# Optimization experiments

Measured on AMD Instinct MI355X. Metric: run time of the kernel, lower is better.

The kernel has to match this reference:

```python
import jax, jax.numpy as jnp
from jax import lax
import numpy as np

CH = 16
STAGES = 6
DN = ('NDHWC', 'DHWIO', 'NDHWC')


def setup_inputs() -> dict:
    key = jax.random.key(0)
    ks = jax.random.split(key, 16)
    B, G = 8, 64
    x = jax.random.normal(ks[0], (B, G, G, G, 1), dtype=jnp.float32)
    mask = jax.random.randint(ks[1], (B, G, G, G), 0, 2, dtype=jnp.int32)
    meta = jax.random.normal(ks[2], (B, 3), dtype=jnp.float32)
    sched = jax.random.normal(ks[3], (B, 128), dtype=jnp.float32)
    s = 0.05
    w_stem = jax.random.normal(ks[4], (5, 5, 5, 1, CH), dtype=jnp.float32) * s
    w_stages = jax.random.normal(ks[5], (STAGES, 3, 3, 3, CH, CH), dtype=jnp.float32) * s
    meta_w1 = jax.random.normal(ks[6], (3, 32), dtype=jnp.float32) * s
    meta_b1 = jnp.zeros((32,), jnp.float32)
    meta_w2 = jax.random.normal(ks[7], (32, 16), dtype=jnp.float32) * s
    meta_b2 = jnp.zeros((16,), jnp.float32)
    mat_w = jax.random.normal(ks[8], (CH * STAGES + 16, 128), dtype=jnp.float32) * s
    mat_b = jnp.zeros((128,), jnp.float32)
    sch_w = jax.random.normal(ks[9], (128, 128), dtype=jnp.float32) * s
    sch_b = jnp.zeros((128,), jnp.float32)
    f1_w = jax.random.normal(ks[10], (256, 128), dtype=jnp.float32) * s
    f1_b = jnp.zeros((128,), jnp.float32)
    f2_w = jax.random.normal(ks[11], (128, 1), dtype=jnp.float32) * s
    f2_b = jnp.zeros((1,), jnp.float32)
    return dict(x=x, mask=mask, meta=meta, sched=sched, w_stem=w_stem,
                w_stages=w_stages, meta_w1=meta_w1, meta_b1=meta_b1,
                meta_w2=meta_w2, meta_b2=meta_b2, mat_w=mat_w, mat_b=mat_b,
                sch_w=sch_w, sch_b=sch_b, f1_w=f1_w, f1_b=f1_b,
                f2_w=f2_w, f2_b=f2_b)


def _pool_mask(m):
    # ME stride-2 output coords = unique(coords // 2): 2x2x2 max-pool, ceil sizes
    return lax.reduce_window(m, jnp.float32(0), lax.max,
                             (1, 2, 2, 2), (1, 2, 2, 2), 'SAME')


def reference(x, mask, meta, sched, w_stem, w_stages, meta_w1, meta_b1,
              meta_w2, meta_b2, mat_w, mat_b, sch_w, sch_b,
              f1_w, f1_b, f2_w, f2_b):
    m = mask.astype(x.dtype)
    feats = x * m[..., None]                       # zero features off-mask
    y = lax.conv_general_dilated(feats, w_stem, (1, 1, 1), 'SAME',
                                 dimension_numbers=DN)
    y = jnp.maximum(y * m[..., None], 0.0)         # stem: conv + mask + ReLU
    pools = []
    for i in range(STAGES):
        y = lax.conv_general_dilated(y, w_stages[i], (2, 2, 2),
                                     [(1, 1), (1, 1), (1, 1)],
                                     dimension_numbers=DN)
        m = _pool_mask(m)
        y = jnp.maximum(y * m[..., None], 0.0)
        denom = jnp.maximum(m.sum(axis=(1, 2, 3)), 1.0)   # occupied voxels
        pools.append(y.sum(axis=(1, 2, 3)) / denom[:, None])
    pools = jnp.concatenate(pools, axis=1)                 # [B, CH*STAGES]
    h = jax.nn.relu(meta[:, :3] @ meta_w1 + meta_b1)
    meta_emb = h @ meta_w2 + meta_b2                        # [B,16]
    m_emb = jax.nn.relu(jnp.concatenate([pools, meta_emb], 1) @ mat_w + mat_b)
    s_emb = jax.nn.relu(sched @ sch_w + sch_b)
    z = jnp.concatenate([m_emb, s_emb], axis=1)             # [B,256]
    z = jax.nn.relu(z @ f1_w + f1_b)
    return z @ f2_w + f2_b                                  # [B,1]
```

## Files before the change

### kernel.cpp

```cpp
#include <hip/hip_runtime.h>

#define CH 16
#define NB 8

typedef unsigned short u16;
typedef unsigned char u8;
typedef unsigned int u32;
typedef __attribute__((ext_vector_type(8))) short s16x8;
typedef __attribute__((ext_vector_type(4))) float f32x4;

__device__ __forceinline__ float bflo(u32 u) { return __uint_as_float(u << 16); }
__device__ __forceinline__ float bfhi(u32 u) { return __uint_as_float(u & 0xffff0000u); }
__device__ __forceinline__ u32 bfrnd(float f) {
  u32 u = __float_as_uint(f);
  return (u + 0x7fffu + ((u >> 16) & 1u)) >> 16;
}
__device__ __forceinline__ u32 packbf_hw(float lo, float hi) {
  u32 r;
  asm("v_cvt_pk_bf16_f32 %0, %1, %2" : "=v"(r) : "v"(lo), "v"(hi));
  return r;
}

__global__ __launch_bounds__(256) void bprep_kernel(
    const float* __restrict__ w_stg, const float* __restrict__ w_stem,
    u16* __restrict__ bpre)
{
  const int e = blockIdx.x * 256 + (int)threadIdx.x;
  if (e >= 4 * 7168 + 3584) return;
  if (e < 4 * 7168) {
    const int s = e / 7168, r0 = e % 7168;
    const int i = r0 >> 9;
    const int r = r0 & 511;
    const int l = r >> 3, j = r & 7;
    const int tap = 2 * i + (l >> 5);
    const int cin = ((l >> 4) & 1) * 8 + j;
    const int n = l & 15;
    const float* w = w_stg + s * 27 * 256;
    const float val = (tap < 27) ? w[(tap * 16 + cin) * 16 + n] : 0.f;
    bpre[s * 7168 + i * 512 + l * 8 + j] = (u16)bfrnd(val);
  } else {
    const int e2 = e - 4 * 7168;
    const int i = e2 >> 9;
    const int r0 = e2 & 511;
    const int lane = r0 >> 3, j = r0 & 7;
    const int quad = lane >> 4, n = lane & 15;
    const int r = i * 4 + quad;
    const float val = (r < 25 && j < 5) ? w_stem[(r * 5 + j) * 16 + n] : 0.f;
    bpre[4 * 7168 + e2] = (u16)bfrnd(val);
  }
}

__global__ __launch_bounds__(256, 6) void stem_mfma(
    const float* __restrict__ x, const int* __restrict__ mask,
    const u16* __restrict__ bpre, u16* __restrict__ yout,
    float* __restrict__ pool_sum, float* __restrict__ cnt)
{
  __shared__ u16 cp[8 * 1168];

  const int b = blockIdx.y;
  const int u = blockIdx.x;
  const int tb = ((u & 7) << 6) | (u >> 3);
  const int z0 = (tb >> 6) * 8;
  const int y0 = ((tb >> 3) & 7) * 8;
  const int x0 = (tb & 7) * 8;
  const int tid = threadIdx.x;

  if (tb == 0) {
    if (tid < 96) pool_sum[b * 96 + tid] = 0.f;
    else if (tid < 102) cnt[b * 6 + (tid - 96)] = 0.f;
  }

  const int lane = tid & 63;
  const int wv = tid >> 6;
  const int n = lane & 15;
  const int quad = lane >> 4;
  const int vy = n >> 2, vx = n & 3;

  s16x8 wf[7];
  {
    const s16x8* wfp = (const s16x8*)(bpre + 4 * 7168);
#pragma unroll
    for (int i = 0; i < 7; ++i) wf[i] = wfp[i * 64 + lane];
  }

  if (tid < 144) {
    const int lz = tid / 12, ly = tid - lz * 12;
    const int gz = z0 + lz - 2, gy = y0 + ly - 2;
    uint4* dst = (uint4*)&cp[tid * 8];
    if ((unsigned)gz < 64u && (unsigned)gy < 64u) {
      const long long rowg =
          ((long long)((b * 64 + gz) * 64 + gy)) * 64 + (x0 - 2);
      float v[12];
      if (rowg >= 0 && rowg + 12 <= (long long)NB * 64 * 64 * 64) {
        const float2* xp = (const float2*)(x + rowg);
        const int2* mp2 = (const int2*)(mask + rowg);
        float2 xv[6]; int2 mv2[6];
#pragma unroll
        for (int j = 0; j < 6; ++j) { xv[j] = xp[j]; mv2[j] = mp2[j]; }
#pragma unroll
        for (int j = 0; j < 6; ++j) {
          v[2 * j]     = xv[j].x * (float)mv2[j].x;
          v[2 * j + 1] = xv[j].y * (float)mv2[j].y;
        }
        if (x0 == 0)  { v[0] = 0.f;  v[1] = 0.f;  }
        if (x0 == 56) { v[10] = 0.f; v[11] = 0.f; }
      } else {
#pragma unroll
        for (int j = 0; j < 12; ++j) {
          const int gx = x0 - 2 + j;
          float vv = 0.f;
          if ((unsigned)gx < 64u) {
            const long long gi = rowg + j;
            vv = x[gi] * (float)mask[gi];
          }
          v[j] = vv;
        }
      }
      const u32 c0 = packbf_hw(v[0], v[1]);
      const u32 c1 = packbf_hw(v[2], v[3]);
      const u32 c2 = packbf_hw(v[4], v[5]);
      const u32 c3 = packbf_hw(v[6], v[7]);
      const u32 c4 = packbf_hw(v[8], v[9]);
      const u32 c5 = packbf_hw(v[10], v[11]);
      const u32 d0 = packbf_hw(v[1], v[2]);
      const u32 d1 = packbf_hw(v[3], v[4]);
      const u32 d2 = packbf_hw(v[5], v[6]);
      const u32 d3 = packbf_hw(v[7], v[8]);
      const u32 d4 = packbf_hw(v[9], v[10]);
      const u32 d5 = packbf_hw(v[11], 0.f);
      dst[0 * 146] = make_uint4(c0, c1, c2, c3);
      dst[1 * 146] = make_uint4(d0, d1, d2, d3);
      dst[2 * 146] = make_uint4(c1, c2, c3, c4);
      dst[3 * 146] = make_uint4(d1, d2, d3, d4);
      dst[4 * 146] = make_uint4(c2, c3, c4, c5);
      dst[5 * 146] = make_uint4(d2, d3, d4, d5);
      dst[6 * 146] = make_uint4(c3, c4, c5, 0u);
      dst[7 * 146] = make_uint4(d3, d4, d5, 0u);
    } else {
#pragma unroll
      for (int p = 0; p < 8; ++p) dst[p * 146] = make_uint4(0u, 0u, 0u, 0u);
    }
  }
  __syncthreads();

  int doff[7];
#pragma unroll
  for (int i = 0; i < 7; ++i) {
    const int r = i * 4 + quad;
    doff[i] = (r < 25) ? ((r / 5) * 12 + (r % 5)) * 8 : 0;
  }
  const int base0 = vx * 1168 + (wv * 12 + vy) * 8;
  const int gi0 = ((b * 64 + z0 + wv) * 64 + y0 + vy) * 64 + x0 + vx;
  u16* outp = yout + (size_t)gi0 * 16 + quad * 4;

  float mvc = (float)mask[gi0];
  for (int s = 0; s < 8; ++s) {
    const int sz = (s >> 2) * 4, sy2 = ((s >> 1) & 1) * 4, sx = (s & 1) * 4;
    const int off = sz * 4096 + sy2 * 64 + sx;
    float mvn = 0.f;
    if (s < 7) {
      const int s1 = s + 1;
      const int offn = ((s1 >> 2) * 4) * 4096 + (((s1 >> 1) & 1) * 4) * 64 +
                       (s1 & 1) * 4;
      mvn = (float)mask[gi0 + offn];
    }
    const int base = base0 + sx * 1168 + (sz * 12 + sy2) * 8;
    f32x4 accA = {0.f, 0.f, 0.f, 0.f};
    f32x4 accB = {0.f, 0.f, 0.f, 0.f};
#pragma unroll
    for (int i = 0; i < 7; ++i) {
      const s16x8 bf = *(const s16x8*)&cp[base + doff[i]];
      if (i & 1)
        accB = __builtin_amdgcn_mfma_f32_16x16x32_bf16(wf[i], bf, accB, 0, 0, 0);
      else
        accA = __builtin_amdgcn_mfma_f32_16x16x32_bf16(wf[i], bf, accA, 0, 0, 0);
    }
    const float f0 = fmaxf(accA[0] + accB[0], 0.f) * mvc;
    const float f1 = fmaxf(accA[1] + accB[1], 0.f) * mvc;
    const float f2 = fmaxf(accA[2] + accB[2], 0.f) * mvc;
    const float f3 = fmaxf(accA[3] + accB[3], 0.f) * mvc;
    *(uint2*)(outp + (size_t)off * 16) =
        make_uint2(packbf_hw(f0, f1), packbf_hw(f2, f3));
    mvc = mvn;
  }
}

template <int S>
__global__ __launch_bounds__(256) void stage_mfma4(
    const u16* __restrict__ yin, const u16* __restrict__ bpre,
    const int* __restrict__ m_in_i, const u8* __restrict__ m_in_u8,
    u16* __restrict__ yout, u8* __restrict__ m_out,
    float* __restrict__ pool_sum, float* __restrict__ cnt,
    const int stage)
{
  __shared__ u16 lb[14 * 512];
  __shared__ float lmp[256];
  __shared__ float lps[4][16];

  constexpr int So = S >> 1;
  constexpr int nvox = So * So * So;
  constexpr int NBX = nvox / 256;
  const int b = blockIdx.y;
  const int tid = threadIdx.x;
  const int u = blockIdx.x;
  int bxi;
  if constexpr (NBX >= 8) bxi = (u & 7) * (NBX / 8) + (u >> 3);
  else bxi = u;
  const int vg0 = bxi * 256;

  {
    const uint4* src = (const uint4*)bpre;
    uint4* dst = (uint4*)lb;
    for (int e = tid; e < 896; e += 256) dst[e] = src[e];
  }

  {
    const int vox = vg0 + tid;
    const int oz = vox / (So * So);
    const int oy = (vox / So) % So;
    const int ox = vox % So;
    float mp = 0.f;
#pragma unroll
    for (int dz = 0; dz < 2; ++dz)
#pragma unroll
      for (int dy = 0; dy < 2; ++dy)
#pragma unroll
        for (int dx = 0; dx < 2; ++dx) {
          const int mi =
              ((b * S + 2 * oz + dz) * S + 2 * oy + dy) * S + 2 * ox + dx;
          const float mv = m_in_i ? (float)m_in_i[mi] : (float)m_in_u8[mi];
          mp = fmaxf(mp, mv);
        }
    lmp[tid] = mp;
  }
  __syncthreads();

  const int wv = tid >> 6;
  const int lane = tid & 63;
  const int m = lane & 15;
  const int quad = lane >> 4;
  const int qh = quad >> 1;
  const int qlo = quad & 1;

  int izb[4], iyb[4], ixb[4];
#pragma unroll
  for (int g = 0; g < 4; ++g) {
    const int vox = vg0 + wv * 64 + g * 16 + m;
    const int oz = vox / (So * So);
    const int oy = (vox / So) % So;
    const int ox = vox % So;
    izb[g] = 2 * oz - 1;
    iyb[g] = 2 * oy - 1;
    ixb[g] = 2 * ox - 1;
  }

  const s16x8* lbv = (const s16x8*)lb;
  f32x4 acc[4];
#pragma unroll
  for (int g = 0; g < 4; ++g) acc[g] = (f32x4){0.f, 0.f, 0.f, 0.f};

#pragma unroll
  for (int i = 0; i < 14; ++i) {
    const int t0 = 2 * i, t1 = 2 * i + 1;
    const int dz0 = t0 / 9, dy0 = (t0 / 3) % 3, dx0 = t0 % 3;
    const int dz1 = (t1 < 27) ? t1 / 9 : 1;
    const int dy1 = (t1 < 27) ? (t1 / 3) % 3 : 1;
    const int dx1 = (t1 < 27) ? t1 % 3 : 1;
    const int dzq = qh ? dz1 : dz0;
    const int dyq = qh ? dy1 : dy0;
    const int dxq = qh ? dx1 : dx0;

    uint4 ar[4];
#pragma unroll
    for (int g = 0; g < 4; ++g) {
      const int iz = izb[g] + dzq;
      const int iy = iyb[g] + dyq;
      const int ix = ixb[g] + dxq;
      const bool valid = (unsigned)iz < (unsigned)S &&
                         (unsigned)iy < (unsigned)S &&
                         (unsigned)ix < (unsigned)S;
      const int izc = min(max(iz, 0), S - 1);
      const int iyc = min(max(iy, 0), S - 1);
      const int ixc = min(max(ix, 0), S - 1);
      const size_t addr =
          (size_t)(((b * S + izc) * S + iyc) * S + ixc) * 16 + qlo * 8;
      uint4 v = *(const uint4*)(yin + addr);
      v.x = valid ? v.x : 0u;
      v.y = valid ? v.y : 0u;
      v.z = valid ? v.z : 0u;
      v.w = valid ? v.w : 0u;
      ar[g] = v;
    }
    const s16x8 bfrag = lbv[i * 64 + lane];
#pragma unroll
    for (int g = 0; g < 4; ++g)
      acc[g] = __builtin_amdgcn_mfma_f32_16x16x32_bf16(
          bfrag, __builtin_bit_cast(s16x8, ar[g]), acc[g], 0, 0, 0);
  }

  {
    float ps0 = 0.f, ps1 = 0.f, ps2 = 0.f, ps3 = 0.f;
#pragma unroll
    for (int g = 0; g < 4; ++g) {
      const int lv = wv * 64 + g * 16 + m;
      const float mp = lmp[lv];
      const float f0 = fmaxf(acc[g][0], 0.f) * mp;
      const float f1 = fmaxf(acc[g][1], 0.f) * mp;
      const float f2 = fmaxf(acc[g][2], 0.f) * mp;
      const float f3 = fmaxf(acc[g][3], 0.f) * mp;
      const size_t gi = (size_t)b * nvox + vg0 + lv;
      *(uint2*)(yout + gi * 16 + quad * 4) =
          make_uint2(packbf_hw(f0, f1), packbf_hw(f2, f3));
      if (quad == 0) m_out[gi] = (u8)mp;
      ps0 += f0; ps1 += f1; ps2 += f2; ps3 += f3;
    }
#pragma unroll
    for (int mm = 1; mm < 16; mm <<= 1) {
      ps0 += __shfl_xor(ps0, mm, 64);
      ps1 += __shfl_xor(ps1, mm, 64);
      ps2 += __shfl_xor(ps2, mm, 64);
      ps3 += __shfl_xor(ps3, mm, 64);
    }
    if (m == 0) {
      lps[wv][quad * 4 + 0] = ps0;
      lps[wv][quad * 4 + 1] = ps1;
      lps[wv][quad * 4 + 2] = ps2;
      lps[wv][quad * 4 + 3] = ps3;
    }
  }
  __syncthreads();
  if (tid < 16) {
    const float s = lps[0][tid] + lps[1][tid] + lps[2][tid] + lps[3][tid];
    atomicAdd(&pool_sum[(b * 6 + stage) * 16 + tid], s);
  } else if (tid == 16) {
    float c = 0.f;
#pragma unroll 16
    for (int v = 0; v < 256; ++v) c += lmp[v];
    atomicAdd(&cnt[b * 6 + stage], c);
  }
}

__global__ __launch_bounds__(256) void tail_kernel(
    const u16* __restrict__ y3g, const u8* __restrict__ m3g,
    const u16* __restrict__ bpre,
    const float* __restrict__ wstg,
    const float* __restrict__ meta, const float* __restrict__ sched,
    const float* __restrict__ mw1, const float* __restrict__ mb1,
    const float* __restrict__ mw2, const float* __restrict__ mb2,
    const float* __restrict__ matw, const float* __restrict__ matb,
    const float* __restrict__ schw, const float* __restrict__ schb,
    const float* __restrict__ f1w, const float* __restrict__ f1b,
    const float* __restrict__ f2w, const float* __restrict__ f2b,
    const float* __restrict__ pool_sum, const float* __restrict__ cnt,
    float* __restrict__ out)
{
  const int b = blockIdx.x;
  const int t = threadIdx.x;
  __shared__ u16 ty3[8192];
  __shared__ float lm3[512];
  __shared__ float pb[4 * 64 * 17];
  __shared__ float ly4[64 * 16];
  __shared__ float lm4[64];
  __shared__ float ps4[256];
  __shared__ float ly5[8 * 16];
  __shared__ float lm5[8];
  __shared__ float ps5[128];
  __shared__ float lsum[3][16];
  __shared__ float lcnt[3];
  __shared__ float invec[112];
  __shared__ float hbuf[32];
  __shared__ float zbuf[256];
  __shared__ float psf[256];
  __shared__ float part[2];

  {
    const uint4* yb = (const uint4*)(y3g + (size_t)b * 8192);
    uint4* dst = (uint4*)ty3;
    for (int i = t; i < 1024; i += 256) dst[i] = yb[i];
    for (int i = t; i < 512; i += 256) lm3[i] = (float)m3g[b * 512 + i];
  }
  __syncthreads();

  {
    const int lane = t & 63;
    const int wv = t >> 6;
    const int mm = lane & 15;
    const int quad = lane >> 4;
    const int qh = quad >> 1, qlo = quad & 1;

    int iz0[4], iy0[4], ix0[4];
#pragma unroll
    for (int g = 0; g < 4; ++g) {
      const int vox = g * 16 + mm;
      iz0[g] = 2 * (vox >> 4) - 1;
      iy0[g] = 2 * ((vox >> 2) & 3) - 1;
      ix0[g] = 2 * (vox & 3) - 1;
    }
    f32x4 a3[4];
#pragma unroll
    for (int g = 0; g < 4; ++g) a3[g] = (f32x4){0.f, 0.f, 0.f, 0.f};
    const s16x8* bp3 = (const s16x8*)(bpre + 3 * 7168);
#pragma unroll
    for (int ii = 0; ii < 4; ++ii) {
      const int i = wv * 4 + ii;
      if (i < 14) {
        const int t0 = 2 * i, t1 = 2 * i + 1;
        const int dz0 = t0 / 9, dy0 = (t0 / 3) % 3, dx0 = t0 % 3;
        const int dz1 = (t1 < 27) ? t1 / 9 : 1;
        const int dy1 = (t1 < 27) ? (t1 / 3) % 3 : 1;
        const int dx1 = (t1 < 27) ? t1 % 3 : 1;
        const int dzq = qh ? dz1 : dz0;
        const int dyq = qh ? dy1 : dy0;
        const int dxq = qh ? dx1 : dx0;
        uint4 ar[4];
#pragma unroll
        for (int g = 0; g < 4; ++g) {
          const int iz = iz0[g] + dzq;
          const int iy = iy0[g] + dyq;
          const int ix = ix0[g] + dxq;
          const bool valid = (unsigned)iz < 8u && (unsigned)iy < 8u &&
                             (unsigned)ix < 8u;
          const int izc = min(max(iz, 0), 7);
          const int iyc = min(max(iy, 0), 7);
          const int ixc = min(max(ix, 0), 7);
          const int ad = ((izc * 8 + iyc) * 8 + ixc) * 16 + qlo * 8;
          uint4 v = *(const uint4*)&ty3[ad];
          v.x = valid ? v.x : 0u;
          v.y = valid ? v.y : 0u;
          v.z = valid ? v.z : 0u;
          v.w = valid ? v.w : 0u;
          ar[g] = v;
        }
        const s16x8 bf = bp3[i * 64 + lane];
#pragma unroll
        for (int g = 0; g < 4; ++g)
          a3[g] = __builtin_amdgcn_mfma_f32_16x16x32_bf16(
              __builtin_bit_cast(s16x8, ar[g]), bf, a3[g], 0, 0, 0);
      }
    }
#pragma unroll
    for (int g = 0; g < 4; ++g)
#pragma unroll
      for (int reg = 0; reg < 4; ++reg)
        pb[wv * 1088 + (g * 16 + quad * 4 + reg) * 17 + mm] = a3[g][reg];
  }
  __syncthreads();

  {
    const int vox = t >> 2, cg = (t & 3) * 4;
    const int oz = vox >> 4, oy = (vox >> 2) & 3, ox = vox & 3;
    float mp = 0.f;
#pragma unroll
    for (int dz = 0; dz < 2; ++dz)
#pragma unroll
      for (int dy = 0; dy < 2; ++dy)
#pragma unroll
        for (int dx = 0; dx < 2; ++dx)
          mp = fmaxf(mp, lm3[((2 * oz + dz) * 8 + 2 * oy + dy) * 8 +
                             2 * ox + dx]);
#pragma unroll
    for (int c = 0; c < 4; ++c) {
      const int ch = cg + c;
      const float s = pb[vox * 17 + ch] + pb[1088 + vox * 17 + ch] +
                      pb[2176 + vox * 17 + ch] + pb[3264 + vox * 17 + ch];
      ly4[vox * 16 + ch] = fmaxf(s, 0.f) * mp;
    }
    if (cg == 0) lm4[vox] = mp;
  }
  __syncthreads();

  if (t < 16) {
    float s = 0.f;
#pragma unroll 16
    for (int v = 0; v < 64; ++v) s += ly4[v * 16 + t];
    lsum[0][t] = s;
  } else if (t == 16) {
    float s = 0.f;
#pragma unroll 16
    for (int v = 0; v < 64; ++v) s += lm4[v];
    lcnt[0] = s;
  }
  {
    const float* w = wstg + 4 * 27 * 256;
    const int o = t >> 1, kh = t & 1;
    const int vox4 = o >> 4, co = o & 15;
    const int oz = vox4 >> 2, oy = (vox4 >> 1) & 1, ox = vox4 & 1;
    float acc = 0.f;
#pragma unroll
    for (int tt = 0; tt < 14; ++tt) {
      const int tap = tt + (kh ? 14 : 0);
      if (tap < 27) {
        const int dz = tap / 9, dy = (tap / 3) % 3, dx = tap % 3;
        const int iz = 2 * oz + dz - 1, iy = 2 * oy + dy - 1,
                  ix = 2 * ox + dx - 1;
        const float s = ((unsigned)iz < 4u && (unsigned)iy < 4u &&
                         (unsigned)ix < 4u) ? 1.f : 0.f;
        const int idx = ((min(max(iz, 0), 3) * 4 + min(max(iy, 0), 3)) * 4 +
                         min(max(ix, 0), 3)) * 16;
        const float* wp = w + tap * 256 + co;
#pragma unroll
        for (int ci = 0; ci < 16; ++ci)
          acc = fmaf(ly4[idx + ci] * s, wp[ci * 16], acc);
      }
    }
    ps4[t] = acc;
  }
  __syncthreads();

  if (t < 128) {
    const int vox4 = t >> 4, co = t & 15;
    float mp = 0.f;
#pragma unroll
    for (int dz = 0; dz < 2; ++dz)
#pragma unroll
      for (int dy = 0; dy < 2; ++dy)
#pragma unroll
        for (int dx = 0; dx < 2; ++dx)
          mp = fmaxf(mp, lm4[((2 * (vox4 >> 2) + dz) * 4 +
                              2 * ((vox4 >> 1) & 1) + dy) * 4 +
                             2 * (vox4 & 1) + dx]);
    ly5[t] = fmaxf(ps4[2 * t] + ps4[2 * t + 1], 0.f) * mp;
    if (co == 0) lm5[vox4] = mp;
  }
  __syncthreads();

  if (t < 16) {
    float s = 0.f;
#pragma unroll
    for (int v = 0; v < 8; ++v) s += ly5[v * 16 + t];
    lsum[1][t] = s;
  } else if (t == 16) {
    lcnt[1] = lm5[0] + lm5[1] + lm5[2] + lm5[3] + lm5[4] + lm5[5] + lm5[6] +
              lm5[7];
  }
  if (t < 128) {
    const float* w = wstg + 5 * 27 * 256;
    const int co = t & 15, k8 = t >> 4;
    float acc = 0.f;
#pragma unroll
    for (int tt = 0; tt < 4; ++tt) {
      const int tap = k8 * 4 + tt;
      if (tap < 27) {
        const int dz = tap / 9, dy = (tap / 3) % 3, dx = tap % 3;
        const int iz = dz - 1, iy = dy - 1, ix = dx - 1;
        const float s = ((unsigned)iz < 2u && (unsigned)iy < 2u &&
                         (unsigned)ix < 2u) ? 1.f : 0.f;
        const int idx = ((min(max(iz, 0), 1) * 2 + min(max(iy, 0), 1)) * 2 +
                         min(max(ix, 0), 1)) * 16;
        const float* wp = w + tap * 256 + co;
#pragma unroll
        for (int ci = 0; ci < 16; ++ci)
          acc = fmaf(ly5[idx + ci] * s, wp[ci * 16], acc);
      }
    }
    ps5[t] = acc;
  }
  __syncthreads();

  if (t < 16) {
    float s = ps5[t] + ps5[16 + t] + ps5[32 + t] + ps5[48 + t] +
              ps5[64 + t] + ps5[80 + t] + ps5[96 + t] + ps5[112 + t];
    float mp = 0.f;
#pragma unroll
    for (int v = 0; v < 8; ++v) mp = fmaxf(mp, lm5[v]);
    lsum[2][t] = fmaxf(s, 0.f) * mp;
    if (t == 0) lcnt[2] = mp;
  } else if (t >= 96 && t < 128) {
    const int j = t - 96;
    float h = mb1[j];
#pragma unroll
    for (int k = 0; k < 3; ++k) h = fmaf(meta[b * 3 + k], mw1[k * 32 + j], h);
    hbuf[j] = fmaxf(h, 0.f);
  }
  __syncthreads();

  if (t < 48) {
    const int s = t >> 4;
    invec[t] = pool_sum[b * 96 + t] / fmaxf(cnt[b * 6 + s], 1.f);
  } else if (t < 96) {
    const int s = (t >> 4) - 3;
    invec[t] = lsum[s][t & 15] / fmaxf(lcnt[s], 1.f);
  } else if (t < 112) {
    const int j = t - 96;
    float e = mb2[j];
#pragma unroll
    for (int k = 0; k < 32; ++k) e = fmaf(hbuf[k], mw2[k * 16 + j], e);
    invec[t] = e;
  }
  __syncthreads();

  if (t < 128) {
    float a = matb[t];
#pragma unroll 16
    for (int k = 0; k < 112; ++k) a = fmaf(invec[k], matw[k * 128 + t], a);
    zbuf[t] = fmaxf(a, 0.f);
  } else {
    const int c = t - 128;
    float s = schb[c];
#pragma unroll 16
    for (int k = 0; k < 128; ++k)
      s = fmaf(sched[b * 128 + k], schw[k * 128 + c], s);
    zbuf[128 + c] = fmaxf(s, 0.f);
  }
  __syncthreads();

  {
    const int col = t & 127, kh = t >> 7;
    float a = 0.f;
#pragma unroll 16
    for (int kk = 0; kk < 128; ++kk) {
      const int k = kh * 128 + kk;
      a = fmaf(zbuf[k], f1w[k * 128 + col], a);
    }
    psf[t] = a;
  }
  __syncthreads();

  if (t < 128) {
    const float a = psf[t] + psf[128 + t] + f1b[t];
    float v = fmaxf(a, 0.f) * f2w[t];
#pragma unroll
    for (int off = 32; off > 0; off >>= 1) v += __shfl_xor(v, off, 64);
    if ((t & 63) == 0) part[t >> 6] = v;
  }
  __syncthreads();
  if (t == 0) out[b] = part[0] + part[1] + f2b[0];
}

extern "C" void kernel_launch(void* const* d_in, const int* in_sizes, int n_in,
                              void* d_out, int out_size, void* d_ws,
                              size_t ws_size, hipStream_t stream)
{
  (void)in_sizes; (void)n_in; (void)out_size; (void)ws_size;
  const float* x      = (const float*)d_in[0];
  const int*   mask   = (const int*)  d_in[1];
  const float* meta   = (const float*)d_in[2];
  const float* sched  = (const float*)d_in[3];
  const float* w_stem = (const float*)d_in[4];
  const float* w_stg  = (const float*)d_in[5];
  const float* mw1    = (const float*)d_in[6];
  const float* mb1    = (const float*)d_in[7];
  const float* mw2    = (const float*)d_in[8];
  const float* mb2    = (const float*)d_in[9];
  const float* matw   = (const float*)d_in[10];
  const float* matb   = (const float*)d_in[11];
  const float* schw   = (const float*)d_in[12];
  const float* schb   = (const float*)d_in[13];
  const float* f1w    = (const float*)d_in[14];
  const float* f1b    = (const float*)d_in[15];
  const float* f2w    = (const float*)d_in[16];
  const float* f2b    = (const float*)d_in[17];
  float* out = (float*)d_out;

  char* ws = (char*)d_ws;
  size_t off = 0;
  auto alloc = [&](size_t nbytes) -> void* {
    void* p = ws + off;
    off += (nbytes + 255) & ~(size_t)255;
    return p;
  };

  u16* y0 = (u16*)alloc((size_t)NB * 64 * 64 * 64 * CH * 2);
  u16* y1 = (u16*)alloc((size_t)NB * 32 * 32 * 32 * CH * 2);
  u16* y2 = (u16*)alloc((size_t)NB * 16 * 16 * 16 * CH * 2);
  u16* y3 = (u16*)alloc((size_t)NB * 8 * 8 * 8 * CH * 2);
  u8* m1 = (u8*)alloc((size_t)NB * 32 * 32 * 32);
  u8* m2 = (u8*)alloc((size_t)NB * 16 * 16 * 16);
  u8* m3 = (u8*)alloc((size_t)NB * 8 * 8 * 8);
  float* pool_sum = (float*)alloc((NB * 96 + NB * 6) * 4);
  float* cnt = pool_sum + NB * 96;
  u16* bpre = (u16*)alloc((4 * 7168 + 3584) * 2);

  bprep_kernel<<<126, 256, 0, stream>>>(w_stg, w_stem, bpre);

  stem_mfma<<<dim3(512, NB), 256, 0, stream>>>(x, mask, bpre, y0,
                                               pool_sum, cnt);

  stage_mfma4<64><<<dim3(128, NB), 256, 0, stream>>>(
      y0, bpre + 0 * 7168, mask, (const u8*)nullptr, y1, m1,
      pool_sum, cnt, 0);
  stage_mfma4<32><<<dim3(16, NB), 256, 0, stream>>>(
      y1, bpre + 1 * 7168, (const int*)nullptr, m1, y2, m2,
      pool_sum, cnt, 1);
  stage_mfma4<16><<<dim3(2, NB), 256, 0, stream>>>(
      y2, bpre + 2 * 7168, (const int*)nullptr, m2, y3, m3,
      pool_sum, cnt, 2);

  tail_kernel<<<NB, 256, 0, stream>>>(y3, m3, bpre, w_stg, meta, sched,
                                      mw1, mb1, mw2, mb2, matw, matb,
                                      schw, schb, f1w, f1b, f2w, f2b,
                                      pool_sum, cnt, out);
}
```

Measured before the change: 194.6 us.

## Fuse stage-2 convolution into tail kernel and drop its separate launch

Stage 2 (16^3 to 8^3 strided conv, pooling, mask pool) now runs inside the per-batch tail kernel. Its output goes straight into shared memory instead of through global y3/m3 buffers, which removes one kernel launch and a global round trip. The tradeoff is parallelism: the stage-2 work that previously ran on 16 blocks now runs on 8 blocks of 256 threads, each handling 512 voxels serially. The stem loop also gets an unroll-2 pragma.

```diff
diff --git a/kernel.cpp b/kernel.cpp
--- a/kernel.cpp
+++ b/kernel.cpp
@@ -154,6 +154,7 @@
   u16* outp = yout + (size_t)gi0 * 16 + quad * 4;
 
   float mvc = (float)mask[gi0];
+#pragma unroll 2
   for (int s = 0; s < 8; ++s) {
     const int sz = (s >> 2) * 4, sy2 = ((s >> 1) & 1) * 4, sx = (s & 1) * 4;
     const int off = sz * 4096 + sy2 * 64 + sx;
@@ -341,7 +342,7 @@
 }
 
 __global__ __launch_bounds__(256) void tail_kernel(
-    const u16* __restrict__ y3g, const u8* __restrict__ m3g,
+    const u16* __restrict__ y2g, const u8* __restrict__ m2g,
     const u16* __restrict__ bpre,
     const float* __restrict__ wstg,
     const float* __restrict__ meta, const float* __restrict__ sched,
@@ -365,29 +366,130 @@
   __shared__ float ly5[8 * 16];
   __shared__ float lm5[8];
   __shared__ float ps5[128];
-  __shared__ float lsum[3][16];
-  __shared__ float lcnt[3];
+  __shared__ float lsum[4][16];
+  __shared__ float lcnt[4];
+  __shared__ float lps2[4][16];
+  __shared__ float lcw[4];
   __shared__ float invec[112];
   __shared__ float hbuf[32];
   __shared__ float zbuf[256];
   __shared__ float psf[256];
   __shared__ float part[2];
 
-  {
-    const uint4* yb = (const uint4*)(y3g + (size_t)b * 8192);
-    uint4* dst = (uint4*)ty3;
-    for (int i = t; i < 1024; i += 256) dst[i] = yb[i];
-    for (int i = t; i < 512; i += 256) lm3[i] = (float)m3g[b * 512 + i];
-  }
-  __syncthreads();
-
-  {
-    const int lane = t & 63;
-    const int wv = t >> 6;
-    const int mm = lane & 15;
-    const int quad = lane >> 4;
-    const int qh = quad >> 1, qlo = quad & 1;
-
+  const int lane = t & 63;
+  const int wv = t >> 6;
+  const int mm = lane & 15;
+  const int quad = lane >> 4;
+  const int qh = quad >> 1, qlo = quad & 1;
+
+  {
+    const s16x8* bp2 = (const s16x8*)(bpre + 2 * 7168);
+    float ps0 = 0.f, ps1 = 0.f, ps2 = 0.f, ps3 = 0.f;
+    float cmask = 0.f;
+#pragma unroll
+    for (int p = 0; p < 2; ++p) {
+      const int vg0 = p * 256;
+      {
+        const int vox = vg0 + t;
+        const int oz = vox >> 6, oy = (vox >> 3) & 7, ox = vox & 7;
+        float mp = 0.f;
+#pragma unroll
+        for (int dz = 0; dz < 2; ++dz)
+#pragma unroll
+          for (int dy = 0; dy < 2; ++dy)
+#pragma unroll
+            for (int dx = 0; dx < 2; ++dx)
+              mp = fmaxf(mp, (float)m2g[((b * 16 + 2 * oz + dz) * 16 +
+                                         2 * oy + dy) * 16 + 2 * ox + dx]);
+        lm3[vox] = mp;
+        cmask += mp;
+      }
+      int izb[4], iyb[4], ixb[4];
+#pragma unroll
+      for (int g = 0; g < 4; ++g) {
+        const int vox = vg0 + wv * 64 + g * 16 + mm;
+        izb[g] = 2 * (vox >> 6) - 1;
+        iyb[g] = 2 * ((vox >> 3) & 7) - 1;
+        ixb[g] = 2 * (vox & 7) - 1;
+      }
+      f32x4 acc[4];
+#pragma unroll
+      for (int g = 0; g < 4; ++g) acc[g] = (f32x4){0.f, 0.f, 0.f, 0.f};
+#pragma unroll
+      for (int i = 0; i < 14; ++i) {
+        const int t0 = 2 * i, t1 = 2 * i + 1;
+        const int dz0 = t0 / 9, dy0 = (t0 / 3) % 3, dx0 = t0 % 3;
+        const int dz1 = (t1 < 27) ? t1 / 9 : 1;
+        const int dy1 = (t1 < 27) ? (t1 / 3) % 3 : 1;
+        const int dx1 = (t1 < 27) ? t1 % 3 : 1;
+        const int dzq = qh ? dz1 : dz0;
+        const int dyq = qh ? dy1 : dy0;
+        const int dxq = qh ? dx1 : dx0;
+        uint4 ar[4];
+#pragma unroll
+        for (int g = 0; g < 4; ++g) {
+          const int iz = izb[g] + dzq;
+          const int iy = iyb[g] + dyq;
+          const int ix = ixb[g] + dxq;
+          const bool valid = (unsigned)iz < 16u && (unsigned)iy < 16u &&
+                             (unsigned)ix < 16u;
+          const int izc = min(max(iz, 0), 15);
+          const int iyc = min(max(iy, 0), 15);
+          const int ixc = min(max(ix, 0), 15);
+          const size_t addr =
+              (size_t)(((b * 16 + izc) * 16 + iyc) * 16 + ixc) * 16 + qlo * 8;
+          uint4 v = *(const uint4*)(y2g + addr);
+          v.x = valid ? v.x : 0u;
+          v.y = valid ? v.y : 0u;
+          v.z = valid ? v.z : 0u;
+          v.w = valid ? v.w : 0u;
+          ar[g] = v;
+        }
+        const s16x8 bfrag = bp2[i * 64 + lane];
+#pragma unroll
+        for (int g = 0; g < 4; ++g)
+          acc[g] = __builtin_amdgcn_mfma_f32_16x16x32_bf16(
+              bfrag, __builtin_bit_cast(s16x8, ar[g]), acc[g], 0, 0, 0);
+      }
+      __syncthreads();
+#pragma unroll
+      for (int g = 0; g < 4; ++g) {
+        const int lv = vg0 + wv * 64 + g * 16 + mm;
+        const float mp = lm3[lv];
+        const float f0 = fmaxf(acc[g][0], 0.f) * mp;
+        const float f1 = fmaxf(acc[g][1], 0.f) * mp;
+        const float f2 = fmaxf(acc[g][2], 0.f) * mp;
+        const float f3 = fmaxf(acc[g][3], 0.f) * mp;
+        *(uint2*)&ty3[lv * 16 + quad * 4] =
+            make_uint2(packbf_hw(f0, f1), packbf_hw(f2, f3));
+        ps0 += f0; ps1 += f1; ps2 += f2; ps3 += f3;
+      }
+    }
+#pragma unroll
+    for (int s = 1; s < 16; s <<= 1) {
+      ps0 += __shfl_xor(ps0, s, 64);
+      ps1 += __shfl_xor(ps1, s, 64);
+      ps2 += __shfl_xor(ps2, s, 64);
+      ps3 += __shfl_xor(ps3, s, 64);
+    }
+    if (mm == 0) {
+      lps2[wv][quad * 4 + 0] = ps0;
+      lps2[wv][quad * 4 + 1] = ps1;
+      lps2[wv][quad * 4 + 2] = ps2;
+      lps2[wv][quad * 4 + 3] = ps3;
+    }
+#pragma unroll
+    for (int s = 1; s < 64; s <<= 1) cmask += __shfl_xor(cmask, s, 64);
+    if (lane == 0) lcw[wv] = cmask;
+  }
+  __syncthreads();
+  if (t < 16) {
+    lsum[0][t] = lps2[0][t] + lps2[1][t] + lps2[2][t] + lps2[3][t];
+  } else if (t == 16) {
+    lcnt[0] = lcw[0] + lcw[1] + lcw[2] + lcw[3];
+  }
+
+  {
     int iz0[4], iy0[4], ix0[4];
 #pragma unroll
     for (int g = 0; g < 4; ++g) {
@@ -473,12 +575,12 @@
     float s = 0.f;
 #pragma unroll 16
     for (int v = 0; v < 64; ++v) s += ly4[v * 16 + t];
-    lsum[0][t] = s;
+    lsum[1][t] = s;
   } else if (t == 16) {
     float s = 0.f;
 #pragma unroll 16
     for (int v = 0; v < 64; ++v) s += lm4[v];
-    lcnt[0] = s;
+    lcnt[1] = s;
   }
   {
     const float* w = wstg + 4 * 27 * 256;
@@ -528,9 +630,9 @@
     float s = 0.f;
 #pragma unroll
     for (int v = 0; v < 8; ++v) s += ly5[v * 16 + t];
-    lsum[1][t] = s;
+    lsum[2][t] = s;
   } else if (t == 16) {
-    lcnt[1] = lm5[0] + lm5[1] + lm5[2] + lm5[3] + lm5[4] + lm5[5] + lm5[6] +
+    lcnt[2] = lm5[0] + lm5[1] + lm5[2] + lm5[3] + lm5[4] + lm5[5] + lm5[6] +
               lm5[7];
   }
   if (t < 128) {
@@ -563,8 +665,8 @@
     float mp = 0.f;
 #pragma unroll
     for (int v = 0; v < 8; ++v) mp = fmaxf(mp, lm5[v]);
-    lsum[2][t] = fmaxf(s, 0.f) * mp;
-    if (t == 0) lcnt[2] = mp;
+    lsum[3][t] = fmaxf(s, 0.f) * mp;
+    if (t == 0) lcnt[3] = mp;
   } else if (t >= 96 && t < 128) {
     const int j = t - 96;
     float h = mb1[j];
@@ -574,11 +676,11 @@
   }
   __syncthreads();
 
-  if (t < 48) {
+  if (t < 32) {
     const int s = t >> 4;
     invec[t] = pool_sum[b * 96 + t] / fmaxf(cnt[b * 6 + s], 1.f);
   } else if (t < 96) {
-    const int s = (t >> 4) - 3;
+    const int s = (t >> 4) - 2;
     invec[t] = lsum[s][t & 15] / fmaxf(lcnt[s], 1.f);
   } else if (t < 112) {
     const int j = t - 96;
@@ -663,10 +765,8 @@
   u16* y0 = (u16*)alloc((size_t)NB * 64 * 64 * 64 * CH * 2);
   u16* y1 = (u16*)alloc((size_t)NB * 32 * 32 * 32 * CH * 2);
   u16* y2 = (u16*)alloc((size_t)NB * 16 * 16 * 16 * CH * 2);
-  u16* y3 = (u16*)alloc((size_t)NB * 8 * 8 * 8 * CH * 2);
   u8* m1 = (u8*)alloc((size_t)NB * 32 * 32 * 32);
   u8* m2 = (u8*)alloc((size_t)NB * 16 * 16 * 16);
-  u8* m3 = (u8*)alloc((size_t)NB * 8 * 8 * 8);
   float* pool_sum = (float*)alloc((NB * 96 + NB * 6) * 4);
   float* cnt = pool_sum + NB * 96;
   u16* bpre = (u16*)alloc((4 * 7168 + 3584) * 2);
@@ -682,11 +782,8 @@
   stage_mfma4<32><<<dim3(16, NB), 256, 0, stream>>>(
       y1, bpre + 1 * 7168, (const int*)nullptr, m1, y2, m2,
       pool_sum, cnt, 1);
-  stage_mfma4<16><<<dim3(2, NB), 256, 0, stream>>>(
-      y2, bpre + 2 * 7168, (const int*)nullptr, m2, y3, m3,
-      pool_sum, cnt, 2);
-
-  tail_kernel<<<NB, 256, 0, stream>>>(y3, m3, bpre, w_stg, meta, sched,
+
+  tail_kernel<<<NB, 256, 0, stream>>>(y2, m2, bpre, w_stg, meta, sched,
                                       mw1, mb1, mw2, mb2, matw, matb,
                                       schw, schb, f1w, f1b, f2w, f2b,
                                       pool_sum, cnt, out);
```

After: 190.3 us. 2.2% less time.
